# Performance work log

Hardware: AMD Instinct MI355X
Metric: run time of the kernel (lower is better)

## Reference

```python
import jax, jax.numpy as jnp
import numpy as np

B, N, F_IN, F_OUT, OUT = 32, 1024, 128, 128, 1


def setup_inputs() -> dict:
    key = jax.random.key(0)
    k = jax.random.split(key, 6)
    A = jax.random.uniform(k[0], (B, N, N), dtype=jnp.float32)
    H = jax.random.normal(k[1], (B, N, F_IN), dtype=jnp.float32)
    W = jax.random.normal(k[2], (F_IN, F_OUT), dtype=jnp.float32)
    b = jax.random.normal(k[3], (F_OUT,), dtype=jnp.float32)
    fc_w = jax.random.normal(k[4], (OUT, F_OUT), dtype=jnp.float32)
    fc_b = jax.random.normal(k[5], (OUT,), dtype=jnp.float32)
    return {"A": A, "H": H, "W": W, "b": b, "fc_w": fc_w, "fc_b": fc_b}


def reference(A, H, W, b, fc_w, fc_b):
    n = A.shape[1]
    A_tilde = A + jnp.eye(n, dtype=A.dtype)          # [B,N,N] add self-loops
    d = jnp.sum(A_tilde, axis=1)                      # [B,N] degrees (col sums, matches torch dim=1)
    inv_sqrt_d = 1.0 / jnp.sqrt(d)                    # elementwise, equivalent to sqrt(inv(diag(d)))
    # D^-1/2 A_tilde D^-1/2 as row/col scaling (avoids diag_embed + matrix inverse)
    A_norm = inv_sqrt_d[:, :, None] * A_tilde * inv_sqrt_d[:, None, :]
    h = jax.nn.relu(jnp.einsum('bij,bjf,fo->bio', A_norm, H, W) + b)  # GCN layer
    pooled = jnp.sum(h, axis=1)                       # [B,F_OUT] sum pooling over nodes
    return pooled @ fc_w.T + fc_b                     # [B,OUT]
```

## Files before the change

### kernel.cpp

```cpp
#include <hip/hip_runtime.h>
#include <hip/hip_bf16.h>

#define NB 32
#define NN 1024
#define FF 128

typedef __attribute__((ext_vector_type(8))) short short8;
typedef __attribute__((ext_vector_type(4))) float f32x4;

static __device__ __forceinline__ unsigned short f2bf(float x) {
  unsigned int u = __float_as_uint(x);
  u += 0x7fffu + ((u >> 16) & 1u);
  return (unsigned short)(u >> 16);
}

static __device__ __forceinline__ unsigned long long pack4bf(float a, float b, float c, float d) {
  return (unsigned long long)f2bf(a)
       | ((unsigned long long)f2bf(b) << 16)
       | ((unsigned long long)f2bf(c) << 32)
       | ((unsigned long long)f2bf(d) << 48);
}

static __device__ __forceinline__ void gl16(const void* g, void* l) {
  __builtin_amdgcn_global_load_lds((const __attribute__((address_space(1))) void*)g,
                                   (__attribute__((address_space(3))) void*)l, 16, 0, 0);
}

__global__ __launch_bounds__(256) void k1_colsum_cvt(const float* __restrict__ A,
                                                     unsigned short* __restrict__ Ab,
                                                     float* __restrict__ partial) {
  int t = threadIdx.x;
  int s = blockIdx.x;
  int b = blockIdx.y;
  const float* base = A + (size_t)b * NN * NN + (size_t)(s * 64) * NN + (t << 2);
  unsigned short* obase = Ab + (size_t)b * NN * NN + (size_t)(s * 64) * NN + (t << 2);
  int jj = t << 2;
  bool diag_band = ((t >> 4) == s);
  float4 sum = make_float4(0.f, 0.f, 0.f, 0.f);
  #pragma unroll 8
  for (int i = 0; i < 64; ++i) {
    float4 v = *reinterpret_cast<const float4*>(base + (size_t)i * NN);
    if (diag_band) {
      int gi = (s << 6) + i;
      v.x += (gi == jj)     ? 1.f : 0.f;
      v.y += (gi == jj + 1) ? 1.f : 0.f;
      v.z += (gi == jj + 2) ? 1.f : 0.f;
      v.w += (gi == jj + 3) ? 1.f : 0.f;
    }
    sum.x += v.x; sum.y += v.y; sum.z += v.z; sum.w += v.w;
    *reinterpret_cast<unsigned long long*>(obase + (size_t)i * NN) =
        pack4bf(v.x, v.y, v.z, v.w);
  }
  *reinterpret_cast<float4*>(partial + (((b << 4) + s) << 10) + jj) = sum;
}

__global__ void k2_finalize(const float* __restrict__ partial, const float* __restrict__ W,
                            float* __restrict__ isd, float* __restrict__ pooled,
                            unsigned short* __restrict__ Wt) {
  int idx = blockIdx.x * 256 + threadIdx.x;
  int b = idx >> 10, j = idx & 1023;
  float d = 0.0f;
  #pragma unroll
  for (int s = 0; s < 16; ++s) d += partial[(((b << 4) + s) << 10) + j];
  isd[idx] = rsqrtf(d);
  if (idx < 4096) pooled[idx] = 0.f;
  if (idx < 16384) {
    int o = idx >> 7, k = idx & 127;
    Wt[idx] = f2bf(W[k * FF + o]);
  }
}

__global__ __launch_bounds__(512) void k3_hw(const float* __restrict__ H,
                                             const unsigned short* __restrict__ Wt,
                                             const float* __restrict__ isd,
                                             unsigned short* __restrict__ HWpT) {
  __shared__ unsigned short Ws[128][136];
  __shared__ unsigned short Hs[128][136];
  int jblk = blockIdx.x;
  int b = blockIdx.y;
  int tid = threadIdx.x, wave = tid >> 6, lane = tid & 63;

  {
    int r = tid >> 4, c = (tid & 15) << 3;
    #pragma unroll
    for (int p = 0; p < 4; ++p) {
      int row = r + (p << 5);
      *reinterpret_cast<short8*>(&Ws[row][c]) =
          *reinterpret_cast<const short8*>(Wt + row * FF + c);
    }
  }
  {
    int r = tid >> 5, c = (tid & 31) << 2;
    const float* Hbase = H + (size_t)b * NN * FF + (size_t)(jblk * 128) * FF;
    #pragma unroll
    for (int p = 0; p < 8; ++p) {
      int row = r + (p << 4);
      const float4 v = *reinterpret_cast<const float4*>(Hbase + (size_t)row * FF + c);
      *reinterpret_cast<unsigned long long*>(&Hs[row][c]) = pack4bf(v.x, v.y, v.z, v.w);
    }
  }
  __syncthreads();

  f32x4 acc[8];
  #pragma unroll
  for (int i = 0; i < 8; ++i) acc[i] = (f32x4){0.f, 0.f, 0.f, 0.f};

  int mrow = (wave << 4) + (lane & 15);
  int koff = (lane >> 4) << 3;
  #pragma unroll
  for (int kk = 0; kk < 4; ++kk) {
    short8 af = *reinterpret_cast<const short8*>(&Ws[mrow][(kk << 5) + koff]);
    #pragma unroll
    for (int nf = 0; nf < 8; ++nf) {
      short8 bf = *reinterpret_cast<const short8*>(&Hs[(nf << 4) + (lane & 15)][(kk << 5) + koff]);
      acc[nf] = __builtin_amdgcn_mfma_f32_16x16x32_bf16(af, bf, acc[nf], 0, 0, 0);
    }
  }

  int q = lane >> 4, l15 = lane & 15;
  #pragma unroll
  for (int nf = 0; nf < 8; ++nf) {
    int jl = (nf << 4) + l15;
    float sc = isd[(b << 10) + (jblk << 7) + jl];
    #pragma unroll
    for (int r = 0; r < 4; ++r) {
      Ws[(wave << 4) + (q << 2) + r][jl] = f2bf(acc[nf][r] * sc);
    }
  }
  __syncthreads();
  {
    unsigned short* obase = HWpT + (size_t)b * FF * NN + (size_t)(jblk * 128);
    int c8 = (tid & 15) << 3;
    #pragma unroll
    for (int p = 0; p < 4; ++p) {
      int o = (p << 5) + (tid >> 4);
      *reinterpret_cast<short8*>(obase + (size_t)o * NN + c8) =
          *reinterpret_cast<const short8*>(&Ws[o][c8]);
    }
  }
}

__global__ __launch_bounds__(256) void k4_gcn(const unsigned short* __restrict__ Ab,
                                              const unsigned short* __restrict__ HWpT,
                                              const float* __restrict__ isd,
                                              const float* __restrict__ bias,
                                              float* __restrict__ pooled) {
  __shared__ __align__(1024) char ldsA[3 * 16384];
  int fid = blockIdx.x;
  int nid = (fid & 7) * 32 + (fid >> 3);
  int b = nid >> 3, iblk = nid & 7;
  int i0 = iblk << 7;
  int tid = threadIdx.x, wave = tid >> 6, lane = tid & 63;
  int wm = wave >> 1, wn = wave & 1;
  int l15 = lane & 15, q = lane >> 4;
  int q16 = q << 4;

  int r8 = lane >> 3;
  int ch = (lane & 7) ^ r8;
  const unsigned short* aS = Ab + (size_t)b * NN * NN
                           + (size_t)(i0 + (wave << 5) + r8) * NN + (ch << 3);
  char* aD0 = ldsA + (wave << 12);

  const unsigned short* bS = HWpT + (size_t)b * FF * NN
                           + (size_t)((wn << 6) + l15) * NN + (q << 3);

  f32x4 acc[4][4];
  #pragma unroll
  for (int m = 0; m < 4; ++m)
    #pragma unroll
    for (int n = 0; n < 4; ++n) acc[m][n] = (f32x4){0.f, 0.f, 0.f, 0.f};

  int swzR = (l15 & 7) << 4;
  int offA[4];
  #pragma unroll
  for (int mr = 0; mr < 4; ++mr)
    offA[mr] = ((wm << 6) + (mr << 4) + l15) * 128 + q16;

  short8 breg[2][4][2];

#define STAGE_A(buf, k0) { \
    const unsigned short* s_ = aS + (k0); \
    char* d_ = ldsA + (buf) * 16384 + (wave << 12); \
    gl16(s_,           d_); \
    gl16(s_ + 8 * NN,  d_ + 1024); \
    gl16(s_ + 16 * NN, d_ + 2048); \
    gl16(s_ + 24 * NN, d_ + 3072); }

#define LOAD_B(slot, k0) { \
    _Pragma("unroll") \
    for (int nf_ = 0; nf_ < 4; ++nf_) { \
      _Pragma("unroll") \
      for (int kk_ = 0; kk_ < 2; ++kk_) \
        breg[slot][nf_][kk_] = *reinterpret_cast<const short8*>( \
            bS + (size_t)(nf_ << 4) * NN + (k0) + (kk_ << 5)); } }

  STAGE_A(0, 0)
  STAGE_A(1, 64)
  LOAD_B(0, 0)

  #pragma unroll
  for (int t = 0; t < 16; ++t) {
    if (t < 15) LOAD_B((t + 1) & 1, (t + 1) * 64)
    if (t < 14) STAGE_A((t + 2) % 3, (t + 2) * 64)
    if (t < 14)      asm volatile("s_waitcnt vmcnt(16)" ::: "memory");
    else if (t == 14) asm volatile("s_waitcnt vmcnt(12)" ::: "memory");
    else              asm volatile("s_waitcnt vmcnt(0)" ::: "memory");
    __builtin_amdgcn_s_barrier();
    const char* Abuf = ldsA + (t % 3) * 16384;
    #pragma unroll
    for (int kk = 0; kk < 2; ++kk) {
      short8 af[4];
      #pragma unroll
      for (int mr = 0; mr < 4; ++mr)
        af[mr] = *reinterpret_cast<const short8*>(Abuf + ((offA[mr] + (kk << 6)) ^ swzR));
      #pragma unroll
      for (int mr = 0; mr < 4; ++mr)
        #pragma unroll
        for (int nf = 0; nf < 4; ++nf)
          acc[mr][nf] = __builtin_amdgcn_mfma_f32_16x16x32_bf16(
              af[mr], breg[t & 1][nf][kk], acc[mr][nf], 0, 0, 0);
    }
    __builtin_amdgcn_s_barrier();
  }
#undef STAGE_A
#undef LOAD_B

  #pragma unroll
  for (int nf = 0; nf < 4; ++nf) {
    int f = (wn << 6) + (nf << 4) + l15;
    float bi = bias[f];
    float stot = 0.f;
    #pragma unroll
    for (int mr = 0; mr < 4; ++mr) {
      int irow = i0 + (wm << 6) + (mr << 4) + (q << 2);
      const f32x4 sc = *reinterpret_cast<const f32x4*>(isd + (b << 10) + irow);
      stot += fmaxf(acc[mr][nf][0] * sc[0] + bi, 0.f)
            + fmaxf(acc[mr][nf][1] * sc[1] + bi, 0.f)
            + fmaxf(acc[mr][nf][2] * sc[2] + bi, 0.f)
            + fmaxf(acc[mr][nf][3] * sc[3] + bi, 0.f);
    }
    stot += __shfl_xor(stot, 16);
    stot += __shfl_xor(stot, 32);
    if (lane < 16) atomicAdd(&pooled[(b << 7) + f], stot);
  }
}

__global__ void k5_out(const float* __restrict__ pooled, const float* __restrict__ fcw,
                       const float* __restrict__ fcb, float* __restrict__ out) {
  int b = blockIdx.x, t = threadIdx.x;
  float s = pooled[(b << 7) + t] * fcw[t] + pooled[(b << 7) + 64 + t] * fcw[64 + t];
  #pragma unroll
  for (int off = 1; off < 64; off <<= 1) s += __shfl_xor(s, off);
  if (t == 0) out[b] = s + fcb[0];
}

extern "C" void kernel_launch(void* const* d_in, const int* in_sizes, int n_in,
                              void* d_out, int out_size, void* d_ws, size_t ws_size,
                              hipStream_t stream) {
  const float* A    = (const float*)d_in[0];
  const float* H    = (const float*)d_in[1];
  const float* W    = (const float*)d_in[2];
  const float* bias = (const float*)d_in[3];
  const float* fcw  = (const float*)d_in[4];
  const float* fcb  = (const float*)d_in[5];
  float* out = (float*)d_out;

  float* ws = (float*)d_ws;
  float* partial = ws;
  float* isd     = ws + 524288;
  float* pooled  = ws + 524288 + 32768;
  unsigned short* Wt   = (unsigned short*)(ws + 524288 + 32768 + 4096);
  unsigned short* HWpT = Wt + 16384;
  unsigned short* Ab   = HWpT + (size_t)NB * FF * NN;

  k1_colsum_cvt<<<dim3(16, 32), 256, 0, stream>>>(A, Ab, partial);
  k2_finalize  <<<128, 256, 0, stream>>>(partial, W, isd, pooled, Wt);
  k3_hw        <<<dim3(8, 32), 512, 0, stream>>>(H, Wt, isd, HWpT);
  k4_gcn       <<<256, 256, 0, stream>>>(Ab, HWpT, isd, bias, pooled);
  k5_out       <<<32, 64, 0, stream>>>(pooled, fcw, fcb, out);
}
```

Before: 73.20 us.

## Fold finalize kernel into consumers, halve GCN tile rows, replace atomics with partials

```diff
diff --git a/kernel.cpp b/kernel.cpp
--- a/kernel.cpp
+++ b/kernel.cpp
@@ -54,40 +54,32 @@
   *reinterpret_cast<float4*>(partial + (((b << 4) + s) << 10) + jj) = sum;
 }
 
-__global__ void k2_finalize(const float* __restrict__ partial, const float* __restrict__ W,
-                            float* __restrict__ isd, float* __restrict__ pooled,
-                            unsigned short* __restrict__ Wt) {
-  int idx = blockIdx.x * 256 + threadIdx.x;
-  int b = idx >> 10, j = idx & 1023;
-  float d = 0.0f;
-  #pragma unroll
-  for (int s = 0; s < 16; ++s) d += partial[(((b << 4) + s) << 10) + j];
-  isd[idx] = rsqrtf(d);
-  if (idx < 4096) pooled[idx] = 0.f;
-  if (idx < 16384) {
-    int o = idx >> 7, k = idx & 127;
-    Wt[idx] = f2bf(W[k * FF + o]);
-  }
-}
-
 __global__ __launch_bounds__(512) void k3_hw(const float* __restrict__ H,
-                                             const unsigned short* __restrict__ Wt,
-                                             const float* __restrict__ isd,
+                                             const float* __restrict__ W,
+                                             const float* __restrict__ partial,
                                              unsigned short* __restrict__ HWpT) {
   __shared__ unsigned short Ws[128][136];
   __shared__ unsigned short Hs[128][136];
+  __shared__ float isdJ[128];
   int jblk = blockIdx.x;
   int b = blockIdx.y;
   int tid = threadIdx.x, wave = tid >> 6, lane = tid & 63;
 
-  {
-    int r = tid >> 4, c = (tid & 15) << 3;
-    #pragma unroll
-    for (int p = 0; p < 4; ++p) {
-      int row = r + (p << 5);
-      *reinterpret_cast<short8*>(&Ws[row][c]) =
-          *reinterpret_cast<const short8*>(Wt + row * FF + c);
-    }
+  if (tid < 128) {
+    float d = 0.f;
+    #pragma unroll
+    for (int s = 0; s < 16; ++s) d += partial[(((b << 4) + s) << 10) + (jblk << 7) + tid];
+    isdJ[tid] = rsqrtf(d);
+  }
+  #pragma unroll
+  for (int p = 0; p < 8; ++p) {
+    int idx = (p << 11) + (tid << 2);
+    int k = idx >> 7, o = idx & 127;
+    const float4 w = *reinterpret_cast<const float4*>(W + idx);
+    Ws[o    ][k] = f2bf(w.x);
+    Ws[o + 1][k] = f2bf(w.y);
+    Ws[o + 2][k] = f2bf(w.z);
+    Ws[o + 3][k] = f2bf(w.w);
   }
   {
     int r = tid >> 5, c = (tid & 31) << 2;
@@ -118,10 +110,11 @@
   }
 
   int q = lane >> 4, l15 = lane & 15;
+  __syncthreads();
   #pragma unroll
   for (int nf = 0; nf < 8; ++nf) {
     int jl = (nf << 4) + l15;
-    float sc = isd[(b << 10) + (jblk << 7) + jl];
+    float sc = isdJ[jl];
     #pragma unroll
     for (int r = 0; r < 4; ++r) {
       Ws[(wave << 4) + (q << 2) + r][jl] = f2bf(acc[nf][r] * sc);
@@ -142,49 +135,54 @@
 
 __global__ __launch_bounds__(256) void k4_gcn(const unsigned short* __restrict__ Ab,
                                               const unsigned short* __restrict__ HWpT,
-                                              const float* __restrict__ isd,
+                                              const float* __restrict__ partial,
                                               const float* __restrict__ bias,
-                                              float* __restrict__ pooled) {
-  __shared__ __align__(1024) char ldsA[3 * 16384];
+                                              float* __restrict__ pooled_part) {
+  __shared__ __align__(1024) char ldsA[3 * 8192];
+  __shared__ __align__(16) float ldsIsd[64];
+  __shared__ float ldsRed[2][128];
   int fid = blockIdx.x;
-  int nid = (fid & 7) * 32 + (fid >> 3);
-  int b = nid >> 3, iblk = nid & 7;
-  int i0 = iblk << 7;
+  int nid = (fid & 7) * 64 + (fid >> 3);
+  int b = nid >> 4, iblk = nid & 15;
+  int i0 = iblk << 6;
   int tid = threadIdx.x, wave = tid >> 6, lane = tid & 63;
   int wm = wave >> 1, wn = wave & 1;
   int l15 = lane & 15, q = lane >> 4;
   int q16 = q << 4;
 
+  if (tid < 64) {
+    float d = 0.f;
+    #pragma unroll
+    for (int s = 0; s < 16; ++s) d += partial[(((b << 4) + s) << 10) + i0 + tid];
+    ldsIsd[tid] = rsqrtf(d);
+  }
+
   int r8 = lane >> 3;
   int ch = (lane & 7) ^ r8;
   const unsigned short* aS = Ab + (size_t)b * NN * NN
-                           + (size_t)(i0 + (wave << 5) + r8) * NN + (ch << 3);
-  char* aD0 = ldsA + (wave << 12);
-
+                           + (size_t)(i0 + (wave << 4) + r8) * NN + (ch << 3);
   const unsigned short* bS = HWpT + (size_t)b * FF * NN
                            + (size_t)((wn << 6) + l15) * NN + (q << 3);
 
-  f32x4 acc[4][4];
-  #pragma unroll
-  for (int m = 0; m < 4; ++m)
+  f32x4 acc[2][4];
+  #pragma unroll
+  for (int m = 0; m < 2; ++m)
     #pragma unroll
     for (int n = 0; n < 4; ++n) acc[m][n] = (f32x4){0.f, 0.f, 0.f, 0.f};
 
   int swzR = (l15 & 7) << 4;
-  int offA[4];
-  #pragma unroll
-  for (int mr = 0; mr < 4; ++mr)
-    offA[mr] = ((wm << 6) + (mr << 4) + l15) * 128 + q16;
+  int offA[2];
+  #pragma unroll
+  for (int mr = 0; mr < 2; ++mr)
+    offA[mr] = ((wm << 5) + (mr << 4) + l15) * 128 + q16;
 
   short8 breg[2][4][2];
 
 #define STAGE_A(buf, k0) { \
     const unsigned short* s_ = aS + (k0); \
-    char* d_ = ldsA + (buf) * 16384 + (wave << 12); \
-    gl16(s_,           d_); \
-    gl16(s_ + 8 * NN,  d_ + 1024); \
-    gl16(s_ + 16 * NN, d_ + 2048); \
-    gl16(s_ + 24 * NN, d_ + 3072); }
+    char* d_ = ldsA + (buf) * 8192 + (wave << 11); \
+    gl16(s_,          d_); \
+    gl16(s_ + 8 * NN, d_ + 1024); }
 
 #define LOAD_B(slot, k0) { \
     _Pragma("unroll") \
@@ -195,26 +193,26 @@
             bS + (size_t)(nf_ << 4) * NN + (k0) + (kk_ << 5)); } }
 
   STAGE_A(0, 0)
+  LOAD_B(0, 0)
   STAGE_A(1, 64)
-  LOAD_B(0, 0)
 
   #pragma unroll
   for (int t = 0; t < 16; ++t) {
     if (t < 15) LOAD_B((t + 1) & 1, (t + 1) * 64)
     if (t < 14) STAGE_A((t + 2) % 3, (t + 2) * 64)
-    if (t < 14)      asm volatile("s_waitcnt vmcnt(16)" ::: "memory");
-    else if (t == 14) asm volatile("s_waitcnt vmcnt(12)" ::: "memory");
+    if (t < 14)       asm volatile("s_waitcnt vmcnt(12)" ::: "memory");
+    else if (t == 14) asm volatile("s_waitcnt vmcnt(10)" ::: "memory");
     else              asm volatile("s_waitcnt vmcnt(0)" ::: "memory");
     __builtin_amdgcn_s_barrier();
-    const char* Abuf = ldsA + (t % 3) * 16384;
+    const char* Abuf = ldsA + (t % 3) * 8192;
     #pragma unroll
     for (int kk = 0; kk < 2; ++kk) {
-      short8 af[4];
+      short8 af[2];
       #pragma unroll
-      for (int mr = 0; mr < 4; ++mr)
+      for (int mr = 0; mr < 2; ++mr)
         af[mr] = *reinterpret_cast<const short8*>(Abuf + ((offA[mr] + (kk << 6)) ^ swzR));
       #pragma unroll
-      for (int mr = 0; mr < 4; ++mr)
+      for (int mr = 0; mr < 2; ++mr)
         #pragma unroll
         for (int nf = 0; nf < 4; ++nf)
           acc[mr][nf] = __builtin_amdgcn_mfma_f32_16x16x32_bf16(
@@ -231,9 +229,8 @@
     float bi = bias[f];
     float stot = 0.f;
     #pragma unroll
-    for (int mr = 0; mr < 4; ++mr) {
-      int irow = i0 + (wm << 6) + (mr << 4) + (q << 2);
-      const f32x4 sc = *reinterpret_cast<const f32x4*>(isd + (b << 10) + irow);
+    for (int mr = 0; mr < 2; ++mr) {
+      const f32x4 sc = *reinterpret_cast<const f32x4*>(&ldsIsd[(wm << 5) + (mr << 4) + (q << 2)]);
       stot += fmaxf(acc[mr][nf][0] * sc[0] + bi, 0.f)
             + fmaxf(acc[mr][nf][1] * sc[1] + bi, 0.f)
             + fmaxf(acc[mr][nf][2] * sc[2] + bi, 0.f)
@@ -241,14 +238,22 @@
     }
     stot += __shfl_xor(stot, 16);
     stot += __shfl_xor(stot, 32);
-    if (lane < 16) atomicAdd(&pooled[(b << 7) + f], stot);
-  }
-}
-
-__global__ void k5_out(const float* __restrict__ pooled, const float* __restrict__ fcw,
+    if (lane < 16) ldsRed[wm][f] = stot;
+  }
+  __syncthreads();
+  if (tid < 128)
+    pooled_part[(((b << 4) + iblk) << 7) + tid] = ldsRed[0][tid] + ldsRed[1][tid];
+}
+
+__global__ void k5_out(const float* __restrict__ pp, const float* __restrict__ fcw,
                        const float* __restrict__ fcb, float* __restrict__ out) {
   int b = blockIdx.x, t = threadIdx.x;
-  float s = pooled[(b << 7) + t] * fcw[t] + pooled[(b << 7) + 64 + t] * fcw[64 + t];
+  float s = 0.f;
+  #pragma unroll
+  for (int slot = 0; slot < 16; ++slot) {
+    const float* p = pp + (((b << 4) + slot) << 7);
+    s += p[t] * fcw[t] + p[t + 64] * fcw[t + 64];
+  }
   #pragma unroll
   for (int off = 1; off < 64; off <<= 1) s += __shfl_xor(s, off);
   if (t == 0) out[b] = s + fcb[0];
@@ -266,16 +271,13 @@
   float* out = (float*)d_out;
 
   float* ws = (float*)d_ws;
-  float* partial = ws;
-  float* isd     = ws + 524288;
-  float* pooled  = ws + 524288 + 32768;
-  unsigned short* Wt   = (unsigned short*)(ws + 524288 + 32768 + 4096);
-  unsigned short* HWpT = Wt + 16384;
+  float* partial     = ws;
+  float* pooled_part = ws + 524288;
+  unsigned short* HWpT = (unsigned short*)(ws + 524288 + 65536);
   unsigned short* Ab   = HWpT + (size_t)NB * FF * NN;
 
   k1_colsum_cvt<<<dim3(16, 32), 256, 0, stream>>>(A, Ab, partial);
-  k2_finalize  <<<128, 256, 0, stream>>>(partial, W, isd, pooled, Wt);
-  k3_hw        <<<dim3(8, 32), 512, 0, stream>>>(H, Wt, isd, HWpT);
-  k4_gcn       <<<256, 256, 0, stream>>>(Ab, HWpT, isd, bias, pooled);
-  k5_out       <<<32, 64, 0, stream>>>(pooled, fcw, fcb, out);
-}
+  k3_hw        <<<dim3(8, 32), 512, 0, stream>>>(H, W, partial, HWpT);
+  k4_gcn       <<<512, 256, 0, stream>>>(Ab, HWpT, partial, bias, pooled_part);
+  k5_out       <<<32, 64, 0, stream>>>(pooled_part, fcw, fcb, out);
+}
```

Result: slower. 80.54 us (+10.0%).
